# Kernel optimization log

Measured on AMD Instinct MI355X. Metric: run time of the kernel, lower is better.

## Reference

```python
import jax, jax.numpy as jnp
import numpy as np

EMB_DIM = 1024
ATT_DIM = 1024
N_HEADS = 16
HEAD_DIM = ATT_DIM // N_HEADS
ROPE_THETA = 10000.0


def setup_inputs() -> dict:
    key = jax.random.key(0)
    k1, k2, k3 = jax.random.split(key, 3)
    B, S = 2, 2048
    x = jax.random.normal(k1, (B, S, EMB_DIM), dtype=jnp.float32)
    # nn.Linear weights stored as [in, out] for x @ W
    W_qkv = jax.random.normal(k2, (EMB_DIM, 3 * ATT_DIM), dtype=jnp.float32) / np.sqrt(EMB_DIM)
    W_out = jax.random.normal(k3, (ATT_DIM, EMB_DIM), dtype=jnp.float32) / np.sqrt(ATT_DIM)
    return {"x": x, "W_qkv": W_qkv, "W_out": W_out}


def _rope_cos_sin(seq_len, dim, dtype):
    # rotary-embedding-torch: freqs over even indices, repeated interleaved
    inv_freq = 1.0 / (ROPE_THETA ** (jnp.arange(0, dim, 2, dtype=jnp.float32) / dim))
    t = jnp.arange(seq_len, dtype=jnp.float32)
    freqs = t[:, None] * inv_freq[None, :]            # [S, dim/2]
    freqs = jnp.repeat(freqs, 2, axis=-1)             # [S, dim] interleaved
    return jnp.cos(freqs).astype(dtype), jnp.sin(freqs).astype(dtype)


def _rotate_half(x):
    # interleaved pairs: (x0, x1) -> (-x1, x0)
    xr = x.reshape(x.shape[:-1] + (x.shape[-1] // 2, 2))
    x1, x2 = xr[..., 0], xr[..., 1]
    return jnp.stack([-x2, x1], axis=-1).reshape(x.shape)


def _apply_rope(x, cos, sin):
    # x: [B, H, S, D]; cos/sin: [S, D]
    return x * cos[None, None] + _rotate_half(x) * sin[None, None]


def reference(x, W_qkv, W_out):
    B, S, _ = x.shape
    qkv = x @ W_qkv                                   # [B, S, 3*ATT]
    qkv = qkv.reshape(B, S, 3, N_HEADS, HEAD_DIM)
    qkv = jnp.moveaxis(qkv, 3, 1)                     # [B, H, S, 3, D]
    q, k, v = qkv[..., 0, :], qkv[..., 1, :], qkv[..., 2, :]

    cos, sin = _rope_cos_sin(S, HEAD_DIM, x.dtype)
    q = _apply_rope(q, cos, sin)
    k = _apply_rope(k, cos, sin)

    scale = 1.0 / np.sqrt(HEAD_DIM)
    scores = jnp.einsum("bhqd,bhkd->bhqk", q, k) * scale
    attn = jax.nn.softmax(scores, axis=-1)
    out = jnp.einsum("bhqk,bhkd->bhqd", attn, v)      # [B, H, S, D]
    out = jnp.moveaxis(out, 1, 2).reshape(B, S, ATT_DIM)
    return out @ W_out                                # [B, S, EMB_DIM]
```

## Files before the change

kernel.cpp:

```cpp
#include <hip/hip_runtime.h>
#include <cstdint>
#include <cstddef>

typedef unsigned short u16;
typedef __bf16 bf16x8 __attribute__((ext_vector_type(8)));
typedef float f32x4 __attribute__((ext_vector_type(4)));

#define DEVI __device__ __forceinline__

constexpr int SEQ = 2048, NH = 16, HD = 64, EMB = 1024, N3 = 3072, MROWS = 4096;

DEVI u16 f2bf(float f) {
    union { float f; unsigned u; } x; x.f = f;
    unsigned r = (x.u + 0x7fffu + ((x.u >> 16) & 1u)) >> 16;
    return (u16)r;
}

DEVI f32x4 mfma16(bf16x8 a, bf16x8 b, f32x4 c) {
    return __builtin_amdgcn_mfma_f32_16x16x32_bf16(a, b, c, 0, 0, 0);
}

DEVI float exp2_raw(float x) {
    float r;
    asm("v_exp_f32 %0, %1" : "=v"(r) : "v"(x));
    return r;
}

#define GLDS16(g, l)                                                          \
    __builtin_amdgcn_global_load_lds(                                         \
        (__attribute__((address_space(1))) void*)(g),                         \
        (__attribute__((address_space(3))) void*)(l), 16, 0, 0)

__global__ __launch_bounds__(256) void prep_k(const float* __restrict__ x,
                                              const float* __restrict__ wqk,
                                              const float* __restrict__ wo,
                                              u16* __restrict__ xb, u16* __restrict__ wqkvT,
                                              u16* __restrict__ woutT, float2* __restrict__ tab) {
    __shared__ float tile[64][65];
    int bid = blockIdx.x, tid = threadIdx.x;
    if (bid < 4096) {
        int i = bid * 256 + tid;
        float4 v = ((const float4*)x)[i];
        ushort4 o;
        o.x = f2bf(v.x); o.y = f2bf(v.y); o.z = f2bf(v.z); o.w = f2bf(v.w);
        ((ushort4*)xb)[i] = o;
    } else if (bid < 5120) {
        const float* in; u16* out; int N, bx, by;
        if (bid < 4864) { in = wqk; out = wqkvT; N = 3072; int bb = bid - 4096; bx = bb % 48; by = bb / 48; }
        else            { in = wo;  out = woutT; N = 1024; int bb = bid - 4864; bx = bb % 16; by = bb / 16; }
        const int K = 1024;
        int k0 = by * 64, n0 = bx * 64;
        for (int i = 0; i < 16; i++) {
            int idx = i * 256 + tid;
            int r = idx >> 6, c = idx & 63;
            tile[r][c] = in[(size_t)(k0 + r) * N + n0 + c];
        }
        __syncthreads();
        for (int i = 0; i < 16; i++) {
            int idx = i * 256 + tid;
            int n = idx >> 6, k = idx & 63;
            out[(size_t)(n0 + n) * K + k0 + k] = f2bf(tile[k][n]);
        }
    } else {
        int idx = (bid - 5120) * 256 + tid;
        int t = idx >> 5, i = idx & 31;
        double ang = (double)t * pow(10000.0, -(double)i / 32.0);
        tab[idx] = make_float2((float)cos(ang), (float)sin(ang));
    }
}

template <int EPI>
__global__ __launch_bounds__(256) void gemm128_k(const u16* __restrict__ A, const u16* __restrict__ Bt,
                                                 int Kd, int Ncols,
                                                 u16* __restrict__ q_out, u16* __restrict__ k_out,
                                                 u16* __restrict__ v_out,
                                                 const float2* __restrict__ tab,
                                                 float* __restrict__ Cout) {
    __shared__ __align__(16) u16 smem[32768];
    u16* As0 = smem;
    u16* As1 = smem + 8192;
    u16* Bs0 = smem + 16384;
    u16* Bs1 = smem + 24576;
    int tid = threadIdx.x, lane = tid & 63, wv = tid >> 6;
    int wr = wv >> 1, wc = wv & 1;
    int l15 = lane & 15, lg = lane >> 4;
    int swr = l15 & 7;

    int nwg = gridDim.x * gridDim.y;
    int bid = blockIdx.y * gridDim.x + blockIdx.x;
    int swzb = (bid & 7) * (nwg >> 3) + (bid >> 3);
    int bx = swzb % gridDim.x, by = swzb / gridDim.x;
    int brow = by * 128, bcol = bx * 128;

    f32x4 acc[4][4];
    for (int i = 0; i < 4; i++)
        for (int j = 0; j < 4; j++) acc[i][j] = (f32x4){0.f, 0.f, 0.f, 0.f};

    const u16* aptr[4];
    const u16* bptr[4];
#pragma unroll
    for (int i = 0; i < 4; i++) {
        int cidx = i * 256 + tid;
        int rrow = cidx >> 3, c8 = cidx & 7;
        int sw = (c8 ^ (rrow & 7)) * 8;
        aptr[i] = A + (size_t)(brow + rrow) * Kd + sw;
        bptr[i] = Bt + (size_t)(bcol + rrow) * Kd + sw;
    }

    auto stageG = [&](u16* Ad, u16* Bd) {
#pragma unroll
        for (int i = 0; i < 4; i++) {
            GLDS16(aptr[i], Ad + (i * 256 + tid) * 8);
            GLDS16(bptr[i], Bd + (i * 256 + tid) * 8);
            aptr[i] += 64;
            bptr[i] += 64;
        }
    };

    auto computeT = [&](const u16* Ar, const u16* Br) {
#pragma unroll
        for (int kk = 0; kk < 2; kk++) {
            bf16x8 af[4], bf[4];
#pragma unroll
            for (int mi = 0; mi < 4; mi++)
                af[mi] = *(const bf16x8*)&Ar[(wr * 64 + mi * 16 + l15) * 64 +
                                             ((kk * 4 + lg) ^ swr) * 8];
#pragma unroll
            for (int ni = 0; ni < 4; ni++)
                bf[ni] = *(const bf16x8*)&Br[(wc * 64 + ni * 16 + l15) * 64 +
                                             ((kk * 4 + lg) ^ swr) * 8];
#pragma unroll
            for (int mi = 0; mi < 4; mi++)
#pragma unroll
                for (int ni = 0; ni < 4; ni++)
                    acc[mi][ni] = mfma16(af[mi], bf[ni], acc[mi][ni]);
        }
    };

    int nIter = Kd >> 6;
    stageG(As0, Bs0);
    for (int it = 0; it < nIter; it += 2) {
        __syncthreads();
        if (it + 1 < nIter) stageG(As1, Bs1);
        computeT(As0, Bs0);
        __syncthreads();
        if (it + 2 < nIter) stageG(As0, Bs0);
        computeT(As1, Bs1);
    }

    if constexpr (EPI == 0) {
        int c = bcol >> 10;
        int bb = brow >> 11, sbase = brow & 2047;
        int hbase = (bcol & 1023) >> 6;
        if (c == 2) {
            for (int mi = 0; mi < 4; mi++)
                for (int ni = 0; ni < 4; ni++) {
                    int col = wc * 64 + ni * 16 + l15;
                    int d = col & 63, h2 = col >> 6;
                    int s0 = sbase + wr * 64 + mi * 16 + lg * 4;
                    ushort4 pw;
                    pw.x = f2bf(acc[mi][ni][0]);
                    pw.y = f2bf(acc[mi][ni][1]);
                    pw.z = f2bf(acc[mi][ni][2]);
                    pw.w = f2bf(acc[mi][ni][3]);
                    *(ushort4*)&v_out[((size_t)(bb * NH + hbase + h2) * HD + d) * SEQ + s0] = pw;
                }
        } else {
            u16* dst = (c == 0) ? q_out : k_out;
            float sc = (c == 0) ? 0.125f * 1.4426950408889634f : 1.0f;
            u16* ep = smem;
            __syncthreads();
            for (int mi = 0; mi < 4; mi++)
                for (int ni = 0; ni < 4; ni++) {
                    int col = wc * 64 + ni * 16 + l15;
                    int dg = col & 63;
                    for (int r = 0; r < 4; r++) {
                        int rowl = wr * 64 + mi * 16 + lg * 4 + r;
                        int s = sbase + rowl;
                        float val = acc[mi][ni][r];
                        float part = __shfl_xor(val, 1);
                        float2 cs = tab[(s << 5) | (dg >> 1)];
                        float o = (dg & 1) ? (val * cs.x + part * cs.y)
                                           : (val * cs.x - part * cs.y);
                        ep[rowl * 136 + (col ^ ((rowl & 7) << 3))] = f2bf(o * sc);
                    }
                }
            __syncthreads();
#pragma unroll
            for (int p = 0; p < 8; p++) {
                int unit = p * 32 + (tid >> 3);
                int h2 = unit >> 7, s_r = unit & 127, j = tid & 7;
                int cj = (h2 * 8 + j) ^ (s_r & 7);
                uint4 w = *(const uint4*)&ep[s_r * 136 + cj * 8];
                *(uint4*)&dst[(((size_t)(bb * NH + hbase + h2) * SEQ + sbase + s_r) << 6) +
                              j * 8] = w;
            }
        }
    } else {
        for (int mi = 0; mi < 4; mi++)
            for (int ni = 0; ni < 4; ni++) {
                int col = bcol + wc * 64 + ni * 16 + l15;
                for (int r = 0; r < 4; r++) {
                    int row = brow + wr * 64 + mi * 16 + lg * 4 + r;
                    Cout[(size_t)row * Ncols + col] = acc[mi][ni][r];
                }
            }
    }
}

__global__ __launch_bounds__(256, 2) void attn7_k(const u16* __restrict__ Qb,
                                                  const u16* __restrict__ Kb,
                                                  const u16* __restrict__ Vtg,
                                                  u16* __restrict__ Ob) {
    __shared__ __align__(16) u16 Ks[2][64 * 64];
    __shared__ __align__(16) u16 Vs[2][64 * 64];
    __shared__ __align__(16) u16 Pl[4][32 * 72];
    int tid = threadIdx.x, lane = tid & 63, wv = tid >> 6;
    int l15 = lane & 15, lg = lane >> 4;
    int swr = l15 & 7;
    int bh = blockIdx.y, b = bh >> 4, h = bh & 15;
    int qbase = blockIdx.x * 128;
    const size_t base = (size_t)bh * SEQ * HD;

    int c0 = tid, c1 = 256 + tid;
    int r0 = c0 >> 3, s0 = ((c0 & 7) ^ (r0 & 7)) * 8;
    int r1 = c1 >> 3, s1 = ((c1 & 7) ^ (r1 & 7)) * 8;
    const u16* kp0 = Kb + base + r0 * HD + s0;
    const u16* kp1 = Kb + base + r1 * HD + s1;
    const u16* vp0 = Vtg + base + (size_t)r0 * SEQ + s0;
    const u16* vp1 = Vtg + base + (size_t)r1 * SEQ + s1;

    bf16x8 qf[2][2];
#pragma unroll
    for (int u = 0; u < 2; u++)
#pragma unroll
        for (int kt = 0; kt < 2; kt++)
            qf[u][kt] = *(const bf16x8*)&Qb[base + (size_t)(qbase + wv * 32 + u * 16 + l15) * HD +
                                            kt * 32 + lg * 8];

    f32x4 oacc[2][4];
    float Lp[2] = {0.f, 0.f};
#pragma unroll
    for (int u = 0; u < 2; u++)
#pragma unroll
        for (int nt = 0; nt < 4; nt++) oacc[u][nt] = (f32x4){0.f, 0.f, 0.f, 0.f};

    auto stage = [&](int buf) {
        GLDS16(kp0, &Ks[buf][c0 * 8]);
        GLDS16(kp1, &Ks[buf][c1 * 8]);
        GLDS16(vp0, &Vs[buf][c0 * 8]);
        GLDS16(vp1, &Vs[buf][c1 * 8]);
        kp0 += 64 * HD; kp1 += 64 * HD;
        vp0 += 64; vp1 += 64;
    };

    stage(0);

    for (int it = 0; it < 32; ++it) {
        int buf = it & 1;
        __syncthreads();
        if (it < 31) stage(buf ^ 1);

        bf16x8 kf[4][2], vf[4][2];
#pragma unroll
        for (int nt = 0; nt < 4; nt++)
#pragma unroll
            for (int kt = 0; kt < 2; kt++) {
                kf[nt][kt] = *(const bf16x8*)&Ks[buf][(nt * 16 + l15) * 64 +
                                                     ((kt * 4 + lg) ^ swr) * 8];
                vf[nt][kt] = *(const bf16x8*)&Vs[buf][(nt * 16 + l15) * 64 +
                                                     ((kt * 4 + lg) ^ swr) * 8];
            }

#pragma unroll
        for (int u = 0; u < 2; u++) {
            f32x4 sa[4];
            __builtin_amdgcn_s_setprio(1);
#pragma unroll
            for (int nt = 0; nt < 4; nt++) {
                f32x4 z = (f32x4){0.f, 0.f, 0.f, 0.f};
#pragma unroll
                for (int kt = 0; kt < 2; kt++) z = mfma16(kf[nt][kt], qf[u][kt], z);
                sa[nt] = z;
            }
            __builtin_amdgcn_s_setprio(0);
            float ls = 0.f;
#pragma unroll
            for (int nt = 0; nt < 4; nt++) {
                float e0 = exp2_raw(sa[nt][0]), e1 = exp2_raw(sa[nt][1]);
                float e2 = exp2_raw(sa[nt][2]), e3 = exp2_raw(sa[nt][3]);
                ls += (e0 + e1) + (e2 + e3);
                unsigned p01, p23;
                asm("v_cvt_pk_bf16_f32 %0, %1, %2" : "=v"(p01) : "v"(e0), "v"(e1));
                asm("v_cvt_pk_bf16_f32 %0, %1, %2" : "=v"(p23) : "v"(e2), "v"(e3));
                uint2 pw; pw.x = p01; pw.y = p23;
                *(uint2*)&Pl[wv][(u * 16 + l15) * 72 + nt * 16 + lg * 4] = pw;
            }
            Lp[u] += ls;
        }

        bf16x8 pa[2][2];
#pragma unroll
        for (int u = 0; u < 2; u++)
#pragma unroll
            for (int kt = 0; kt < 2; kt++)
                pa[u][kt] = *(const bf16x8*)&Pl[wv][(u * 16 + l15) * 72 + kt * 32 + lg * 8];
        __builtin_amdgcn_s_setprio(1);
#pragma unroll
        for (int kt = 0; kt < 2; kt++)
#pragma unroll
            for (int nt = 0; nt < 4; nt++)
#pragma unroll
                for (int u = 0; u < 2; u++)
                    oacc[u][nt] = mfma16(pa[u][kt], vf[nt][kt], oacc[u][nt]);
        __builtin_amdgcn_s_setprio(0);
    }

    float linv[2][4];
#pragma unroll
    for (int u = 0; u < 2; u++) {
        float L = Lp[u];
        L += __shfl_xor(L, 16);
        L += __shfl_xor(L, 32);
#pragma unroll
        for (int r = 0; r < 4; r++) linv[u][r] = 1.0f / __shfl(L, lg * 4 + r);
    }
#pragma unroll
    for (int u = 0; u < 2; u++)
#pragma unroll
        for (int nt = 0; nt < 4; nt++)
#pragma unroll
            for (int r = 0; r < 4; r++) {
                int row = qbase + wv * 32 + u * 16 + lg * 4 + r;
                Ob[(size_t)(b * SEQ + row) * EMB + h * HD + nt * 16 + l15] =
                    f2bf(oacc[u][nt][r] * linv[u][r]);
            }
}


extern "C" void kernel_launch(void* const* d_in, const int* in_sizes, int n_in,
                              void* d_out, int out_size, void* d_ws, size_t ws_size,
                              hipStream_t stream) {
    const float* x = (const float*)d_in[0];
    const float* wqk = (const float*)d_in[1];
    const float* wo = (const float*)d_in[2];
    float* out = (float*)d_out;
    char* ws = (char*)d_ws;

    u16* xb = (u16*)(ws + 0);
    u16* wqkvT = (u16*)(ws + 8388608);
    u16* woutT = (u16*)(ws + 14680064);
    u16* qb = (u16*)(ws + 16777216);
    u16* kb = (u16*)(ws + 25165824);
    u16* vb = (u16*)(ws + 33554432);
    u16* ao = (u16*)(ws + 41943040);
    float2* tab = (float2*)(ws + 50331648);

    prep_k<<<5376, 256, 0, stream>>>(x, wqk, wo, xb, wqkvT, woutT, tab);
    gemm128_k<0><<<dim3(N3 / 128, MROWS / 128), 256, 0, stream>>>(xb, wqkvT, EMB, N3, qb, kb, vb,
                                                                  tab, nullptr);
    attn7_k<<<dim3(SEQ / 128, 2 * NH), 256, 0, stream>>>(qb, kb, vb, ao);
    gemm128_k<1><<<dim3(EMB / 128, MROWS / 128), 256, 0, stream>>>(ao, woutT, EMB, EMB, nullptr,
                                                                   nullptr, nullptr, nullptr, out);
}
```

Measured before the change: 112.1 us.

## Keep softmax probabilities in registers by permuting K rows to match MFMA layout

Removes the per-wave LDS round trip for the P tile in attention. K rows are loaded in a permuted order, so the S=K·Q MFMA output lanes already hold probabilities in the A-operand layout needed for the P·V MFMA, and packed bf16 values go straight into registers. The LDS swizzle for K and V staging is changed to match the new row mapping. This saves LDS writes, reads and 18KB of shared memory per block, but relies on a correct key-index permutation and may introduce new bank conflicts with the different swizzle.

```diff
diff --git a/kernel.cpp b/kernel.cpp
--- a/kernel.cpp
+++ b/kernel.cpp
@@ -5,6 +5,7 @@
 typedef unsigned short u16;
 typedef __bf16 bf16x8 __attribute__((ext_vector_type(8)));
 typedef float f32x4 __attribute__((ext_vector_type(4)));
+typedef unsigned int u32x4 __attribute__((ext_vector_type(4)));
 
 #define DEVI __device__ __forceinline__
 
@@ -208,23 +209,23 @@
     }
 }
 
-__global__ __launch_bounds__(256, 2) void attn7_k(const u16* __restrict__ Qb,
+__global__ __launch_bounds__(256, 2) void attn8_k(const u16* __restrict__ Qb,
                                                   const u16* __restrict__ Kb,
                                                   const u16* __restrict__ Vtg,
                                                   u16* __restrict__ Ob) {
     __shared__ __align__(16) u16 Ks[2][64 * 64];
     __shared__ __align__(16) u16 Vs[2][64 * 64];
-    __shared__ __align__(16) u16 Pl[4][32 * 72];
     int tid = threadIdx.x, lane = tid & 63, wv = tid >> 6;
     int l15 = lane & 15, lg = lane >> 4;
-    int swr = l15 & 7;
+    int fk = (l15 & 3) | (((l15 >> 2) & 1) << 2);
+    int fv = (l15 & 3) | (((l15 >> 3) & 1) << 2);
     int bh = blockIdx.y, b = bh >> 4, h = bh & 15;
     int qbase = blockIdx.x * 128;
     const size_t base = (size_t)bh * SEQ * HD;
 
     int c0 = tid, c1 = 256 + tid;
-    int r0 = c0 >> 3, s0 = ((c0 & 7) ^ (r0 & 7)) * 8;
-    int r1 = c1 >> 3, s1 = ((c1 & 7) ^ (r1 & 7)) * 8;
+    int r0 = c0 >> 3, s0 = ((c0 & 7) ^ ((r0 & 3) | ((r0 >> 1) & 4))) * 8;
+    int r1 = c1 >> 3, s1 = ((c1 & 7) ^ ((r1 & 3) | ((r1 >> 1) & 4))) * 8;
     const u16* kp0 = Kb + base + r0 * HD + s0;
     const u16* kp1 = Kb + base + r1 * HD + s1;
     const u16* vp0 = Vtg + base + (size_t)r0 * SEQ + s0;
@@ -263,15 +264,17 @@
 
         bf16x8 kf[4][2], vf[4][2];
 #pragma unroll
-        for (int nt = 0; nt < 4; nt++)
+        for (int nt = 0; nt < 4; nt++) {
+            int rk = ((nt >> 1) << 5) + ((l15 >> 2) << 3) + ((nt & 1) << 2) + (l15 & 3);
 #pragma unroll
             for (int kt = 0; kt < 2; kt++) {
-                kf[nt][kt] = *(const bf16x8*)&Ks[buf][(nt * 16 + l15) * 64 +
-                                                     ((kt * 4 + lg) ^ swr) * 8];
+                kf[nt][kt] = *(const bf16x8*)&Ks[buf][rk * 64 + (((kt * 4 + lg) ^ fk)) * 8];
                 vf[nt][kt] = *(const bf16x8*)&Vs[buf][(nt * 16 + l15) * 64 +
-                                                     ((kt * 4 + lg) ^ swr) * 8];
-            }
-
+                                                     (((kt * 4 + lg) ^ fv)) * 8];
+            }
+        }
+
+        unsigned pk[2][4][2];
 #pragma unroll
         for (int u = 0; u < 2; u++) {
             f32x4 sa[4];
@@ -290,11 +293,8 @@
                 float e0 = exp2_raw(sa[nt][0]), e1 = exp2_raw(sa[nt][1]);
                 float e2 = exp2_raw(sa[nt][2]), e3 = exp2_raw(sa[nt][3]);
                 ls += (e0 + e1) + (e2 + e3);
-                unsigned p01, p23;
-                asm("v_cvt_pk_bf16_f32 %0, %1, %2" : "=v"(p01) : "v"(e0), "v"(e1));
-                asm("v_cvt_pk_bf16_f32 %0, %1, %2" : "=v"(p23) : "v"(e2), "v"(e3));
-                uint2 pw; pw.x = p01; pw.y = p23;
-                *(uint2*)&Pl[wv][(u * 16 + l15) * 72 + nt * 16 + lg * 4] = pw;
+                asm("v_cvt_pk_bf16_f32 %0, %1, %2" : "=v"(pk[u][nt][0]) : "v"(e0), "v"(e1));
+                asm("v_cvt_pk_bf16_f32 %0, %1, %2" : "=v"(pk[u][nt][1]) : "v"(e2), "v"(e3));
             }
             Lp[u] += ls;
         }
@@ -303,8 +303,11 @@
 #pragma unroll
         for (int u = 0; u < 2; u++)
 #pragma unroll
-            for (int kt = 0; kt < 2; kt++)
-                pa[u][kt] = *(const bf16x8*)&Pl[wv][(u * 16 + l15) * 72 + kt * 32 + lg * 8];
+            for (int kt = 0; kt < 2; kt++) {
+                u32x4 t = {pk[u][2 * kt][0], pk[u][2 * kt][1], pk[u][2 * kt + 1][0],
+                           pk[u][2 * kt + 1][1]};
+                pa[u][kt] = __builtin_bit_cast(bf16x8, t);
+            }
         __builtin_amdgcn_s_setprio(1);
 #pragma unroll
         for (int kt = 0; kt < 2; kt++)
@@ -359,7 +362,7 @@
     prep_k<<<5376, 256, 0, stream>>>(x, wqk, wo, xb, wqkvT, woutT, tab);
     gemm128_k<0><<<dim3(N3 / 128, MROWS / 128), 256, 0, stream>>>(xb, wqkvT, EMB, N3, qb, kb, vb,
                                                                   tab, nullptr);
-    attn7_k<<<dim3(SEQ / 128, 2 * NH), 256, 0, stream>>>(qb, kb, vb, ao);
+    attn8_k<<<dim3(SEQ / 128, 2 * NH), 256, 0, stream>>>(qb, kb, vb, ao);
     gemm128_k<1><<<dim3(EMB / 128, MROWS / 128), 256, 0, stream>>>(ao, woutT, EMB, EMB, nullptr,
                                                                    nullptr, nullptr, nullptr, out);
 }
```

Result: faster. 106.5 us (-5.0%).
